# Optimization experiments

Hardware: AMD Instinct MI355X
Metric: run time of the kernel (lower is better)

Reference implementation:

```python
import jax, jax.numpy as jnp
import numpy as np

NH = 8          # num_heads (init kwarg)
NUM_GROUPS = 32
EPS = 1e-5


def setup_inputs() -> dict:
    key = jax.random.key(0)
    ks = jax.random.split(key, 4)
    B, C, H, W = 2, 512, 64, 64
    x = jax.random.normal(ks[0], (B, C, H, W), dtype=jnp.float32)
    qkv_w = jax.random.normal(ks[1], (3 * C, C), dtype=jnp.float32) * (1.0 / np.sqrt(C))
    proj_w = jax.random.normal(ks[2], (C, C), dtype=jnp.float32) * (1.0 / np.sqrt(C))
    proj_b = jax.random.normal(ks[3], (C,), dtype=jnp.float32) * 0.02
    gn_w = jnp.ones((C,), dtype=jnp.float32)
    gn_b = jnp.zeros((C,), dtype=jnp.float32)
    return {"x": x, "qkv_w": qkv_w, "proj_w": proj_w, "proj_b": proj_b,
            "gn_w": gn_w, "gn_b": gn_b}


def _group_norm(x, gamma, beta):
    B, C, H, W = x.shape
    xg = x.reshape(B, NUM_GROUPS, C // NUM_GROUPS, H, W)
    mean = xg.mean(axis=(2, 3, 4), keepdims=True)
    var = xg.var(axis=(2, 3, 4), keepdims=True)
    xg = (xg - mean) * jax.lax.rsqrt(var + EPS)
    x = xg.reshape(B, C, H, W)
    return x * gamma[None, :, None, None] + beta[None, :, None, None]


def reference(x, qkv_w, proj_w, proj_b, gn_w, gn_b):
    B, C, H, W = x.shape
    h = _group_norm(x, gn_w, gn_b)
    # 1x1 conv == channel matmul
    qkv = jnp.einsum('oc,bchw->bohw', qkv_w, h)  # [B, 3C, H, W]
    # faithful legacy reshape: per-head contiguous [q,k,v] blocks of 3*C//NH channels
    qkv = qkv.reshape(B * NH, 3 * C // NH, H * W)
    q, k, v = jnp.split(qkv, 3, axis=1)          # each [B*NH, C//NH, HW]
    scale = 1.0 / np.sqrt(np.sqrt(C // NH))
    attn = jnp.einsum('bci,bcj->bij', q * scale, k * scale)  # [B*NH, HW, HW]
    attn = jax.nn.softmax(attn, axis=-1)
    hout = jnp.einsum('bij,bcj->bci', attn, v)   # [B*NH, C//NH, HW]
    hout = hout.reshape(B, C, H, W)
    hout = jnp.einsum('oc,bchw->bohw', proj_w, hout) + proj_b[None, :, None, None]
    return x + hout
```

## Files before the change

### kernel.cpp

```cpp
#include <hip/hip_runtime.h>
#include <math.h>

typedef __attribute__((ext_vector_type(8))) short short8;
typedef __attribute__((ext_vector_type(4))) short short4v;
typedef __attribute__((ext_vector_type(4))) float floatx4;
typedef __attribute__((ext_vector_type(16))) float floatx16;

__device__ __forceinline__ unsigned short f2bf(float f) {
  union { float f; unsigned int u; } v; v.f = f;
  unsigned int r = v.u + 0x7fffu + ((v.u >> 16) & 1u);
  return (unsigned short)(r >> 16);
}

__device__ __forceinline__ float bf2f(unsigned short h) {
  union { unsigned int u; float f; } v; v.u = ((unsigned int)h) << 16;
  return v.f;
}

__device__ __forceinline__ unsigned int pack2(unsigned short a, unsigned short b) {
  return (unsigned int)a | ((unsigned int)b << 16);
}

__device__ __forceinline__ unsigned int rbits(float f) {
  union { float f; unsigned int u; } v; v.f = f;
  return v.u + 0x8000u;
}

__device__ __forceinline__ float fast_exp2(float x) {
#if __has_builtin(__builtin_amdgcn_exp2f)
  return __builtin_amdgcn_exp2f(x);
#else
  return exp2f(x);
#endif
}

__device__ __forceinline__ void async16(const unsigned short* gp, unsigned short* lp) {
  __builtin_amdgcn_global_load_lds(
      (__attribute__((address_space(1))) void*)(gp),
      (__attribute__((address_space(3))) void*)(lp), 16, 0, 0);
}

__global__ void setup_kernel(const float* __restrict__ x, float* __restrict__ stats,
                             const float* __restrict__ qkv_w, unsigned short* __restrict__ wqkv,
                             const float* __restrict__ proj_w, unsigned short* __restrict__ wproj) {
  if (blockIdx.x < 64) {
    int bg = blockIdx.x;
    const float4* p = (const float4*)(x + (size_t)bg * 65536);
    float s = 0.f, ss = 0.f;
    for (int i = threadIdx.x; i < 16384; i += 256) {
      float4 v = p[i];
      s  += v.x + v.y + v.z + v.w;
      ss += v.x*v.x + v.y*v.y + v.z*v.z + v.w*v.w;
    }
    #pragma unroll
    for (int off = 32; off >= 1; off >>= 1) {
      s  += __shfl_xor(s,  off, 64);
      ss += __shfl_xor(ss, off, 64);
    }
    __shared__ float red[2][4];
    int wv = threadIdx.x >> 6;
    if ((threadIdx.x & 63) == 0) { red[0][wv] = s; red[1][wv] = ss; }
    __syncthreads();
    if (threadIdx.x == 0) {
      s  = red[0][0] + red[0][1] + red[0][2] + red[0][3];
      ss = red[1][0] + red[1][1] + red[1][2] + red[1][3];
      float mean = s * (1.f/65536.f);
      float var  = ss * (1.f/65536.f) - mean*mean;
      stats[2*bg]   = mean;
      stats[2*bg+1] = rsqrtf(var + 1e-5f);
    }
  } else {
    int i = (blockIdx.x - 64) * 256 + threadIdx.x;
    const float* s; unsigned short* d;
    if (i < 196608) { s = qkv_w; d = wqkv; }
    else { i -= 196608; s = proj_w; d = wproj; }
    float4 vv = ((const float4*)s)[i];
    uint2 o;
    o.x = pack2(f2bf(vv.x), f2bf(vv.y));
    o.y = pack2(f2bf(vv.z), f2bf(vv.w));
    ((uint2*)d)[i] = o;
  }
}

__global__ void gn_apply_t(const float* __restrict__ x, const float* __restrict__ stats,
                           const float* __restrict__ gw, const float* __restrict__ gb,
                           unsigned short* __restrict__ h_t) {
  __shared__ __align__(16) unsigned short tile[64][72];
  const int b = blockIdx.z, c0 = blockIdx.y * 64, hw0 = blockIdx.x * 64;
  const int t = threadIdx.x;
  {
    const int cl = t >> 2;
    const int hs = (t & 3) * 16;
    const int c  = c0 + cl;
    const int g  = c >> 4;
    const float mean = stats[2*(b*32 + g)];
    const float rstd = stats[2*(b*32 + g) + 1];
    const float w  = gw[c] * rstd;
    const float bb = gb[c] - mean * w;
    const float4* src = (const float4*)(x + ((size_t)(b*512 + c))*4096 + hw0 + hs);
    #pragma unroll
    for (int i = 0; i < 4; i++) {
      float4 vv = src[i];
      unsigned short* d = &tile[cl][hs + i*4];
      d[0] = f2bf(vv.x*w + bb); d[1] = f2bf(vv.y*w + bb);
      d[2] = f2bf(vv.z*w + bb); d[3] = f2bf(vv.w*w + bb);
    }
  }
  __syncthreads();
  {
    const int hwl = t >> 2;
    const int cs  = (t & 3) * 16;
    uint4 w0, w1;
    w0.x = pack2(tile[cs+ 0][hwl], tile[cs+ 1][hwl]);
    w0.y = pack2(tile[cs+ 2][hwl], tile[cs+ 3][hwl]);
    w0.z = pack2(tile[cs+ 4][hwl], tile[cs+ 5][hwl]);
    w0.w = pack2(tile[cs+ 6][hwl], tile[cs+ 7][hwl]);
    w1.x = pack2(tile[cs+ 8][hwl], tile[cs+ 9][hwl]);
    w1.y = pack2(tile[cs+10][hwl], tile[cs+11][hwl]);
    w1.z = pack2(tile[cs+12][hwl], tile[cs+13][hwl]);
    w1.w = pack2(tile[cs+14][hwl], tile[cs+15][hwl]);
    unsigned short* dst = h_t + ((size_t)(b*4096 + hw0 + hwl))*512 + c0 + cs;
    *(uint4*)dst       = w0;
    *(uint4*)(dst + 8) = w1;
  }
}

__global__ __launch_bounds__(256, 3)
void qkv_gemm(const unsigned short* __restrict__ A,
              const unsigned short* __restrict__ Bt,
              unsigned short* __restrict__ q_t,
              unsigned short* __restrict__ k_t,
              unsigned short* __restrict__ v_) {
  __shared__ __align__(16) unsigned short As[128*32];
  __shared__ __align__(16) unsigned short Bs[128*32];
  const int b   = blockIdx.z;
  const int n0  = blockIdx.x * 128;
  const int o0  = blockIdx.y * 128;
  const int tid = threadIdx.x;
  const int wave = tid >> 6, lane = tid & 63;
  const int wr = wave >> 1, wc = wave & 1;
  const int fm = lane & 15, fq = lane >> 4;
  const int srow = lane >> 2, scol = (lane & 3) * 8;

  const unsigned short* Ab = A + (size_t)o0 * 512;
  const unsigned short* Bb = Bt + ((size_t)b*4096 + n0) * 512;

  bool vsw[4];
  #pragma unroll
  for (int fr = 0; fr < 4; fr++) {
    const int ob = o0 + wr*64 + fr*16;
    vsw[fr] = ((ob % 192) >> 6) == 2;
  }

  floatx4 acc[4][4];
  #pragma unroll
  for (int i = 0; i < 4; i++)
    #pragma unroll
    for (int j = 0; j < 4; j++) acc[i][j] = (floatx4){0.f,0.f,0.f,0.f};

  for (int k0 = 0; k0 < 512; k0 += 32) {
    __syncthreads();
    #pragma unroll
    for (int cc = 0; cc < 2; cc++) {
      int ch = wave*2 + cc;
      async16(Ab + (size_t)(ch*16 + srow)*512 + k0 + scol, &As[ch*512]);
      async16(Bb + (size_t)(ch*16 + srow)*512 + k0 + scol, &Bs[ch*512]);
    }
    __syncthreads();
    short8 af[4], bf[4];
    #pragma unroll
    for (int f = 0; f < 4; f++) {
      af[f] = *(const short8*)&As[(wr*64 + f*16 + fm)*32 + fq*8];
      bf[f] = *(const short8*)&Bs[(wc*64 + f*16 + fm)*32 + fq*8];
    }
    #pragma unroll
    for (int fr = 0; fr < 4; fr++) {
      if (vsw[fr]) {
        #pragma unroll
        for (int fc = 0; fc < 4; fc++)
          acc[fr][fc] = __builtin_amdgcn_mfma_f32_16x16x32_bf16(bf[fc], af[fr], acc[fr][fc], 0, 0, 0);
      } else {
        #pragma unroll
        for (int fc = 0; fc < 4; fc++)
          acc[fr][fc] = __builtin_amdgcn_mfma_f32_16x16x32_bf16(af[fr], bf[fc], acc[fr][fc], 0, 0, 0);
      }
    }
  }

  #pragma unroll
  for (int fr = 0; fr < 4; fr++) {
    const int ob     = o0 + wr*64 + fr*16;
    const int head   = ob / 192;
    const int rem    = ob % 192;
    const int region = rem >> 6;
    const int bhh    = b*8 + head;
    #pragma unroll
    for (int fc = 0; fc < 4; fc++) {
      if (region == 0) {
        const int i = n0 + wc*64 + fc*16 + fm;
        const int dsub = (rem & 63) + fq*4;
        unsigned short t4[4];
        #pragma unroll
        for (int r = 0; r < 4; r++) t4[r] = f2bf(acc[fr][fc][r] * 0.18033688f);
        uint2 o; o.x = pack2(t4[0], t4[1]); o.y = pack2(t4[2], t4[3]);
        *(uint2*)&q_t[((size_t)bhh*4096 + i)*64 + dsub] = o;
      } else if (region == 1) {
        const int i = n0 + wc*64 + fc*16 + fm;
        const int dsub = (rem & 63) + fq*4;
        unsigned short t4[4];
        #pragma unroll
        for (int r = 0; r < 4; r++) t4[r] = f2bf(acc[fr][fc][r]);
        uint2 o; o.x = pack2(t4[0], t4[1]); o.y = pack2(t4[2], t4[3]);
        *(uint2*)&k_t[((size_t)bhh*4096 + i)*64 + dsub] = o;
      } else {
        const int dsub = (rem & 63) + fm;
        const int tok0 = n0 + wc*64 + fc*16 + fq*4;
        unsigned short t4[4];
        #pragma unroll
        for (int r = 0; r < 4; r++) t4[r] = f2bf(acc[fr][fc][r]);
        uint2 o; o.x = pack2(t4[0], t4[1]); o.y = pack2(t4[2], t4[3]);
        *(uint2*)&v_[((size_t)bhh*64 + dsub)*4096 + tok0] = o;
      }
    }
  }
}

__global__ __launch_bounds__(256, 2)
void proj_gemm(const unsigned short* __restrict__ A,
               const unsigned short* __restrict__ Bt,
               float* __restrict__ outp,
               const float* __restrict__ xres,
               const float* __restrict__ pbias) {
  __shared__ __align__(16) unsigned short As[64*32];
  __shared__ __align__(16) unsigned short Bs[128*32];
  const int b   = blockIdx.z;
  const int n0  = blockIdx.x * 128;
  const int o0  = blockIdx.y * 64;
  const int tid = threadIdx.x;
  const int wave = tid >> 6, lane = tid & 63;
  const int wr = wave >> 1, wc = wave & 1;
  const int fm = lane & 15, fq = lane >> 4;
  const int srow = lane >> 2, scol = (lane & 3) * 8;

  const unsigned short* Ab = A + (size_t)o0 * 512;
  const unsigned short* Bb = Bt + ((size_t)b*4096 + n0) * 512;

  floatx4 acc[2][4];
  #pragma unroll
  for (int i = 0; i < 2; i++)
    #pragma unroll
    for (int j = 0; j < 4; j++) acc[i][j] = (floatx4){0.f,0.f,0.f,0.f};

  for (int k0 = 0; k0 < 512; k0 += 32) {
    __syncthreads();
    async16(Ab + (size_t)(wave*16 + srow)*512 + k0 + scol, &As[wave*512]);
    #pragma unroll
    for (int cc = 0; cc < 2; cc++) {
      int ch = wave*2 + cc;
      async16(Bb + (size_t)(ch*16 + srow)*512 + k0 + scol, &Bs[ch*512]);
    }
    __syncthreads();
    short8 af[2], bf[4];
    #pragma unroll
    for (int f = 0; f < 2; f++)
      af[f] = *(const short8*)&As[(wr*32 + f*16 + fm)*32 + fq*8];
    #pragma unroll
    for (int f = 0; f < 4; f++)
      bf[f] = *(const short8*)&Bs[(wc*64 + f*16 + fm)*32 + fq*8];
    #pragma unroll
    for (int fr = 0; fr < 2; fr++)
      #pragma unroll
      for (int fc = 0; fc < 4; fc++)
        acc[fr][fc] = __builtin_amdgcn_mfma_f32_16x16x32_bf16(af[fr], bf[fc], acc[fr][fc], 0, 0, 0);
  }

  #pragma unroll
  for (int fr = 0; fr < 2; fr++)
    #pragma unroll
    for (int fc = 0; fc < 4; fc++) {
      const int i = n0 + wc*64 + fc*16 + fm;
      #pragma unroll
      for (int r = 0; r < 4; r++) {
        const int o = o0 + wr*32 + fr*16 + fq*4 + r;
        const size_t idx = ((size_t)b*512 + o)*4096 + i;
        outp[idx] = xres[idx] + pbias[o] + acc[fr][fc][r];
      }
    }
}

template <int SPLIT>
__global__ __launch_bounds__(256, 2)
void attn_kernel(const unsigned short* __restrict__ q_t,
                 const unsigned short* __restrict__ k_t,
                 const unsigned short* __restrict__ v_,
                 unsigned short* __restrict__ hout_t,
                 unsigned short* __restrict__ o_part,
                 float* __restrict__ l_part) {
  __shared__ __align__(16) unsigned short Ks[2][64*72];
  __shared__ __align__(16) unsigned short Vs[2][64*72];

  const int bh  = blockIdx.x;
  const int q0  = blockIdx.y * 256;
  const int js  = SPLIT ? blockIdx.z : 0;
  const int nit = SPLIT ? 32 : 64;
  const int jbase = js * 2048;
  const int tid = threadIdx.x;
  const int wave = tid >> 6, lane = tid & 63;
  const int ln = lane & 31, h = lane >> 5;

  short8 qf[2][4];
  #pragma unroll
  for (int ih = 0; ih < 2; ih++) {
    const unsigned short* qrow = q_t + ((size_t)bh*4096 + q0 + wave*64 + ih*32 + ln)*64;
    #pragma unroll
    for (int kc = 0; kc < 4; kc++)
      qf[ih][kc] = *(const short8*)(qrow + kc*16 + h*8);
  }

  const floatx16 z16 = {0.f,0.f,0.f,0.f,0.f,0.f,0.f,0.f,
                        0.f,0.f,0.f,0.f,0.f,0.f,0.f,0.f};
  floatx16 o_acc[2][2];
  #pragma unroll
  for (int ih = 0; ih < 2; ih++) { o_acc[ih][0] = z16; o_acc[ih][1] = z16; }
  float l0 = 0.f, l1 = 0.f;

  const int sr = tid >> 3;
  const int sc = (tid & 7) * 8;
  const int cch = tid & 7;
  const int vpos = ((cch >> 2) * 32) + ((cch & 3) * 4);
  const unsigned short* kbase = k_t + (size_t)bh*262144;
  const unsigned short* vbase = v_  + (size_t)bh*262144;

  uint4 kr0 = *(const uint4*)&kbase[(size_t)(jbase + sr)*64 + sc];
  uint4 kr1 = *(const uint4*)&kbase[(size_t)(jbase + sr + 32)*64 + sc];
  uint4 vr0 = *(const uint4*)&vbase[(size_t)sr*4096 + jbase + sc];
  uint4 vr1 = *(const uint4*)&vbase[(size_t)(sr+32)*4096 + jbase + sc];

  for (int it = 0; it < nit; it++) {
    unsigned short* Kc = Ks[it & 1];
    unsigned short* Vc = Vs[it & 1];
    *(uint4*)&Kc[sr*72 + sc]      = kr0;
    *(uint4*)&Kc[(sr+32)*72 + sc] = kr1;
    *(uint2*)&Vc[sr*72 + vpos]           = *(const uint2*)&vr0;
    *(uint2*)&Vc[sr*72 + vpos + 16]      = *((const uint2*)&vr0 + 1);
    *(uint2*)&Vc[(sr+32)*72 + vpos]      = *(const uint2*)&vr1;
    *(uint2*)&Vc[(sr+32)*72 + vpos + 16] = *((const uint2*)&vr1 + 1);
    __syncthreads();

    {
      const int jn = jbase + (((it + 1) & (nit - 1)) * 64);
      kr0 = *(const uint4*)&kbase[(size_t)(jn + sr)*64 + sc];
      kr1 = *(const uint4*)&kbase[(size_t)(jn + sr + 32)*64 + sc];
      vr0 = *(const uint4*)&vbase[(size_t)sr*4096 + jn + sc];
      vr1 = *(const uint4*)&vbase[(size_t)(sr+32)*4096 + jn + sc];
    }

    #pragma unroll
    for (int mj = 0; mj < 2; mj++) {
      short8 kf[4];
      #pragma unroll
      for (int kc = 0; kc < 4; kc++)
        kf[kc] = *(const short8*)&Kc[(mj*32 + ln)*72 + kc*16 + h*8];
      short8 vv[2][2];
      #pragma unroll
      for (int dn = 0; dn < 2; dn++)
        #pragma unroll
        for (int t2 = 0; t2 < 2; t2++)
          vv[dn][t2] = *(const short8*)&Vc[(dn*32 + ln)*72 + mj*32 + h*16 + t2*8];

      #pragma unroll
      for (int ih = 0; ih < 2; ih++) {
        floatx16 st = __builtin_amdgcn_mfma_f32_32x32x16_bf16(kf[0], qf[ih][0], z16, 0, 0, 0);
        #pragma unroll
        for (int kc = 1; kc < 4; kc++)
          st = __builtin_amdgcn_mfma_f32_32x32x16_bf16(kf[kc], qf[ih][kc], st, 0, 0, 0);

        unsigned pk[8];
        float lacc = 0.f;
        #pragma unroll
        for (int rp = 0; rp < 8; rp++) {
          float p0 = fast_exp2(st[2*rp]);
          float p1 = fast_exp2(st[2*rp + 1]);
          lacc += p0 + p1;
          pk[rp] = __builtin_amdgcn_perm(rbits(p1), rbits(p0), 0x07060302u);
        }
        if (ih) l1 += lacc; else l0 += lacc;

        #pragma unroll
        for (int t2 = 0; t2 < 2; t2++) {
          union { unsigned u[2]; short4v s; } a0, a1;
          a0.u[0] = pk[4*t2];     a0.u[1] = pk[4*t2 + 1];
          a1.u[0] = pk[4*t2 + 2]; a1.u[1] = pk[4*t2 + 3];
          #pragma unroll
          for (int dn = 0; dn < 2; dn++) {
            short4v vlo = __builtin_shufflevector(vv[dn][t2], vv[dn][t2], 0, 1, 2, 3);
            short4v vhi = __builtin_shufflevector(vv[dn][t2], vv[dn][t2], 4, 5, 6, 7);
            o_acc[ih][dn] = __builtin_amdgcn_mfma_f32_32x32x8bf16_1k(a0.s, vlo, o_acc[ih][dn], 0, 0, 0);
            o_acc[ih][dn] = __builtin_amdgcn_mfma_f32_32x32x8bf16_1k(a1.s, vhi, o_acc[ih][dn], 0, 0, 0);
          }
        }
      }
    }
  }

  l0 += __shfl_xor(l0, 32, 64);
  l1 += __shfl_xor(l1, 32, 64);

  if (SPLIT) {
    #pragma unroll
    for (int ih = 0; ih < 2; ih++) {
      unsigned short* op = o_part +
          (((size_t)(js*16 + bh)*4096 + q0 + wave*64 + ih*32) * 64);
      #pragma unroll
      for (int r = 0; r < 16; r++) {
        const int il = (r & 3) + 8*(r >> 2) + 4*h;
        op[(size_t)il*64 + ln]      = f2bf(o_acc[ih][0][r]);
        op[(size_t)il*64 + 32 + ln] = f2bf(o_acc[ih][1][r]);
      }
    }
    if (lane < 32) {
      l_part[(size_t)(js*16 + bh)*4096 + q0 + wave*64 + lane]      = l0;
      l_part[(size_t)(js*16 + bh)*4096 + q0 + wave*64 + 32 + lane] = l1;
    }
  } else {
    const float linv0 = 1.f / l0;
    const float linv1 = 1.f / l1;
    const int bb = bh >> 3;
    const int cb = (bh & 7) * 64;
    #pragma unroll
    for (int ih = 0; ih < 2; ih++) {
      #pragma unroll
      for (int r = 0; r < 16; r++) {
        const int il = (r & 3) + 8*(r >> 2) + 4*h;
        const float inv = __shfl(ih ? linv1 : linv0, il, 64);
        const int i = q0 + wave*64 + ih*32 + il;
        unsigned short* dst = &hout_t[((size_t)bb*4096 + i)*512 + cb + ln];
        dst[0]  = f2bf(o_acc[ih][0][r] * inv);
        dst[32] = f2bf(o_acc[ih][1][r] * inv);
      }
    }
  }
}

__global__ void attn_combine(const unsigned short* __restrict__ o_part,
                             const float* __restrict__ l_part,
                             unsigned short* __restrict__ hout_t) {
  const int bh = blockIdx.x;
  const int i0 = blockIdx.y * 64;
  const int t  = threadIdx.x;
  const int d4 = (t & 15) * 4;
  const int il = t >> 4;
  const int bb = bh >> 3;
  const int cb = (bh & 7) * 64;
  const size_t JS = (size_t)16 * 4096 * 64;
  #pragma unroll
  for (int p = 0; p < 4; p++) {
    const int i = i0 + p*16 + il;
    const size_t ob = ((size_t)bh*4096 + i)*64 + d4;
    uint2 a = *(const uint2*)&o_part[ob];
    uint2 b = *(const uint2*)&o_part[ob + JS];
    const size_t lb = (size_t)bh*4096 + i;
    const float inv = 1.f / (l_part[lb] + l_part[lb + 65536]);
    float o0 = (bf2f((unsigned short)(a.x & 0xffff)) + bf2f((unsigned short)(b.x & 0xffff))) * inv;
    float o1 = (bf2f((unsigned short)(a.x >> 16))    + bf2f((unsigned short)(b.x >> 16)))    * inv;
    float o2 = (bf2f((unsigned short)(a.y & 0xffff)) + bf2f((unsigned short)(b.y & 0xffff))) * inv;
    float o3 = (bf2f((unsigned short)(a.y >> 16))    + bf2f((unsigned short)(b.y >> 16)))    * inv;
    uint2 w;
    w.x = pack2(f2bf(o0), f2bf(o1));
    w.y = pack2(f2bf(o2), f2bf(o3));
    *(uint2*)&hout_t[((size_t)bb*4096 + i)*512 + cb + d4] = w;
  }
}

extern "C" void kernel_launch(void* const* d_in, const int* in_sizes, int n_in,
                              void* d_out, int out_size, void* d_ws, size_t ws_size,
                              hipStream_t stream) {
  (void)in_sizes; (void)n_in; (void)out_size;
  const float* x      = (const float*)d_in[0];
  const float* qkv_w  = (const float*)d_in[1];
  const float* proj_w = (const float*)d_in[2];
  const float* proj_b = (const float*)d_in[3];
  const float* gn_w   = (const float*)d_in[4];
  const float* gn_b   = (const float*)d_in[5];
  float* out = (float*)d_out;

  char* ws = (char*)d_ws;
  unsigned short* h_t   = (unsigned short*)(ws);
  unsigned short* q_t   = (unsigned short*)(ws + ((size_t)8  << 20));
  unsigned short* k_t   = (unsigned short*)(ws + ((size_t)16 << 20));
  unsigned short* v_    = (unsigned short*)(ws + ((size_t)24 << 20));
  unsigned short* wqkv  = (unsigned short*)(ws + ((size_t)32 << 20));
  unsigned short* wproj = (unsigned short*)(ws + ((size_t)34 << 20));
  float* stats          = (float*)(ws + ((size_t)35 << 20));
  unsigned short* o_part = (unsigned short*)(ws + ((size_t)36 << 20));
  float* l_part          = (float*)(ws + ((size_t)52 << 20));
  unsigned short* hout_t = h_t;

  const bool split = ws_size >= (((size_t)52 << 20) + ((size_t)1 << 19));

  setup_kernel<<<dim3(1088), dim3(256), 0, stream>>>(x, stats, qkv_w, wqkv, proj_w, wproj);
  gn_apply_t<<<dim3(64, 8, 2), dim3(256), 0, stream>>>(x, stats, gn_w, gn_b, h_t);
  qkv_gemm<<<dim3(32, 12, 2), dim3(256), 0, stream>>>(wqkv, h_t, q_t, k_t, v_);
  if (split) {
    attn_kernel<1><<<dim3(16, 16, 2), dim3(256), 0, stream>>>(q_t, k_t, v_, nullptr,
                                                              o_part, l_part);
    attn_combine<<<dim3(16, 64), dim3(256), 0, stream>>>(o_part, l_part, hout_t);
  } else {
    attn_kernel<0><<<dim3(16, 16), dim3(256), 0, stream>>>(q_t, k_t, v_, hout_t,
                                                           nullptr, nullptr);
  }
  proj_gemm<<<dim3(32, 8, 2), dim3(256), 0, stream>>>(wproj, hout_t, out, x, proj_b);
}
```

Measured before the change: 227.1 us.

## Fuse split-KV attention combine into projection GEMM and raise split count

Removes the separate attn_combine kernel and the non-split attention path. The projection GEMM now reads the partial attention outputs and row sums directly, sums the splits and normalizes while staging its B tile into LDS, and prefetches the next tile's partials into registers. The attention kernel now takes its split count from the grid, using 4 KV splits when the workspace is large enough, and its launch bounds are raised to 4 blocks per CU. This saves one kernel launch and one round-trip of hout through memory, and more splits give more parallel attention blocks. The cost is more partial-output traffic and extra combine work repeated across the 8 output-channel blocks of the projection.

After: 446.3 us. 1.97x slower.

```diff
diff --git a/kernel.cpp b/kernel.cpp
--- a/kernel.cpp
+++ b/kernel.cpp
@@ -12,9 +12,11 @@
   return (unsigned short)(r >> 16);
 }
 
-__device__ __forceinline__ float bf2f(unsigned short h) {
-  union { unsigned int u; float f; } v; v.u = ((unsigned int)h) << 16;
-  return v.f;
+__device__ __forceinline__ float lo16f(unsigned int w) {
+  union { unsigned int u; float f; } v; v.u = w << 16; return v.f;
+}
+__device__ __forceinline__ float hi16f(unsigned int w) {
+  union { unsigned int u; float f; } v; v.u = w & 0xffff0000u; return v.f;
 }
 
 __device__ __forceinline__ unsigned int pack2(unsigned short a, unsigned short b) {
@@ -225,75 +227,10 @@
   }
 }
 
-__global__ __launch_bounds__(256, 2)
-void proj_gemm(const unsigned short* __restrict__ A,
-               const unsigned short* __restrict__ Bt,
-               float* __restrict__ outp,
-               const float* __restrict__ xres,
-               const float* __restrict__ pbias) {
-  __shared__ __align__(16) unsigned short As[64*32];
-  __shared__ __align__(16) unsigned short Bs[128*32];
-  const int b   = blockIdx.z;
-  const int n0  = blockIdx.x * 128;
-  const int o0  = blockIdx.y * 64;
-  const int tid = threadIdx.x;
-  const int wave = tid >> 6, lane = tid & 63;
-  const int wr = wave >> 1, wc = wave & 1;
-  const int fm = lane & 15, fq = lane >> 4;
-  const int srow = lane >> 2, scol = (lane & 3) * 8;
-
-  const unsigned short* Ab = A + (size_t)o0 * 512;
-  const unsigned short* Bb = Bt + ((size_t)b*4096 + n0) * 512;
-
-  floatx4 acc[2][4];
-  #pragma unroll
-  for (int i = 0; i < 2; i++)
-    #pragma unroll
-    for (int j = 0; j < 4; j++) acc[i][j] = (floatx4){0.f,0.f,0.f,0.f};
-
-  for (int k0 = 0; k0 < 512; k0 += 32) {
-    __syncthreads();
-    async16(Ab + (size_t)(wave*16 + srow)*512 + k0 + scol, &As[wave*512]);
-    #pragma unroll
-    for (int cc = 0; cc < 2; cc++) {
-      int ch = wave*2 + cc;
-      async16(Bb + (size_t)(ch*16 + srow)*512 + k0 + scol, &Bs[ch*512]);
-    }
-    __syncthreads();
-    short8 af[2], bf[4];
-    #pragma unroll
-    for (int f = 0; f < 2; f++)
-      af[f] = *(const short8*)&As[(wr*32 + f*16 + fm)*32 + fq*8];
-    #pragma unroll
-    for (int f = 0; f < 4; f++)
-      bf[f] = *(const short8*)&Bs[(wc*64 + f*16 + fm)*32 + fq*8];
-    #pragma unroll
-    for (int fr = 0; fr < 2; fr++)
-      #pragma unroll
-      for (int fc = 0; fc < 4; fc++)
-        acc[fr][fc] = __builtin_amdgcn_mfma_f32_16x16x32_bf16(af[fr], bf[fc], acc[fr][fc], 0, 0, 0);
-  }
-
-  #pragma unroll
-  for (int fr = 0; fr < 2; fr++)
-    #pragma unroll
-    for (int fc = 0; fc < 4; fc++) {
-      const int i = n0 + wc*64 + fc*16 + fm;
-      #pragma unroll
-      for (int r = 0; r < 4; r++) {
-        const int o = o0 + wr*32 + fr*16 + fq*4 + r;
-        const size_t idx = ((size_t)b*512 + o)*4096 + i;
-        outp[idx] = xres[idx] + pbias[o] + acc[fr][fc][r];
-      }
-    }
-}
-
-template <int SPLIT>
-__global__ __launch_bounds__(256, 2)
+__global__ __launch_bounds__(256, 4)
 void attn_kernel(const unsigned short* __restrict__ q_t,
                  const unsigned short* __restrict__ k_t,
                  const unsigned short* __restrict__ v_,
-                 unsigned short* __restrict__ hout_t,
                  unsigned short* __restrict__ o_part,
                  float* __restrict__ l_part) {
   __shared__ __align__(16) unsigned short Ks[2][64*72];
@@ -301,9 +238,9 @@
 
   const int bh  = blockIdx.x;
   const int q0  = blockIdx.y * 256;
-  const int js  = SPLIT ? blockIdx.z : 0;
-  const int nit = SPLIT ? 32 : 64;
-  const int jbase = js * 2048;
+  const int js  = blockIdx.z;
+  const int nit = 64 / gridDim.z;
+  const int jbase = js * nit * 64;
   const int tid = threadIdx.x;
   const int wave = tid >> 6, lane = tid & 63;
   const int ln = lane & 31, h = lane >> 5;
@@ -406,70 +343,145 @@
   l0 += __shfl_xor(l0, 32, 64);
   l1 += __shfl_xor(l1, 32, 64);
 
-  if (SPLIT) {
-    #pragma unroll
-    for (int ih = 0; ih < 2; ih++) {
-      unsigned short* op = o_part +
-          (((size_t)(js*16 + bh)*4096 + q0 + wave*64 + ih*32) * 64);
-      #pragma unroll
-      for (int r = 0; r < 16; r++) {
-        const int il = (r & 3) + 8*(r >> 2) + 4*h;
-        op[(size_t)il*64 + ln]      = f2bf(o_acc[ih][0][r]);
-        op[(size_t)il*64 + 32 + ln] = f2bf(o_acc[ih][1][r]);
+  #pragma unroll
+  for (int ih = 0; ih < 2; ih++) {
+    unsigned short* op = o_part +
+        (((size_t)(js*16 + bh)*4096 + q0 + wave*64 + ih*32) * 64);
+    #pragma unroll
+    for (int r = 0; r < 16; r++) {
+      const int il = (r & 3) + 8*(r >> 2) + 4*h;
+      op[(size_t)il*64 + ln]      = f2bf(o_acc[ih][0][r]);
+      op[(size_t)il*64 + 32 + ln] = f2bf(o_acc[ih][1][r]);
+    }
+  }
+  if (lane < 32) {
+    l_part[(size_t)(js*16 + bh)*4096 + q0 + wave*64 + lane]      = l0;
+    l_part[(size_t)(js*16 + bh)*4096 + q0 + wave*64 + 32 + lane] = l1;
+  }
+}
+
+template <int NS>
+__global__ __launch_bounds__(256, 2)
+void proj_fused(const unsigned short* __restrict__ A,
+                const unsigned short* __restrict__ o_part,
+                const float* __restrict__ l_part,
+                float* __restrict__ outp,
+                const float* __restrict__ xres,
+                const float* __restrict__ pbias) {
+  __shared__ __align__(16) unsigned short As[64*32];
+  __shared__ __align__(16) unsigned short Bs[128*36];
+  __shared__ float Linv[8][128];
+  const int b   = blockIdx.z;
+  const int n0  = blockIdx.x * 128;
+  const int o0  = blockIdx.y * 64;
+  const int tid = threadIdx.x;
+  const int wave = tid >> 6, lane = tid & 63;
+  const int wr = wave >> 1, wc = wave & 1;
+  const int fm = lane & 15, fq = lane >> 4;
+  const int srow = lane >> 2, scol = (lane & 3) * 8;
+  const int tk = tid & 127, hc = tid >> 7;
+
+  #pragma unroll
+  for (int p = 0; p < 4; p++) {
+    const int e = p*256 + tid;
+    const int head = e >> 7, token = e & 127;
+    float s = 0.f;
+    #pragma unroll
+    for (int sp = 0; sp < NS; sp++)
+      s += l_part[((size_t)(sp*16 + b*8 + head)*4096) + n0 + token];
+    Linv[head][token] = 1.f / s;
+  }
+
+  const unsigned short* Ab = A + (size_t)o0 * 512;
+
+  floatx4 acc[2][4];
+  #pragma unroll
+  for (int i = 0; i < 2; i++)
+    #pragma unroll
+    for (int j = 0; j < 4; j++) acc[i][j] = (floatx4){0.f,0.f,0.f,0.f};
+
+  uint4 raw[NS][2];
+  {
+    const int d0 = hc*16;
+    #pragma unroll
+    for (int sp = 0; sp < NS; sp++) {
+      const unsigned short* p = o_part +
+          ((size_t)(sp*16 + b*8)*4096 + n0 + tk)*64 + d0;
+      raw[sp][0] = *(const uint4*)p;
+      raw[sp][1] = *(const uint4*)(p + 8);
+    }
+  }
+
+  for (int k0 = 0; k0 < 512; k0 += 32) {
+    __syncthreads();
+    {
+      const int head = k0 >> 6;
+      const float linv = Linv[head][tk];
+      float fa[16];
+      #pragma unroll
+      for (int j = 0; j < 8; j++) {
+        unsigned w = ((const unsigned*)raw[0])[j];
+        fa[2*j]   = lo16f(w);
+        fa[2*j+1] = hi16f(w);
       }
-    }
-    if (lane < 32) {
-      l_part[(size_t)(js*16 + bh)*4096 + q0 + wave*64 + lane]      = l0;
-      l_part[(size_t)(js*16 + bh)*4096 + q0 + wave*64 + 32 + lane] = l1;
-    }
-  } else {
-    const float linv0 = 1.f / l0;
-    const float linv1 = 1.f / l1;
-    const int bb = bh >> 3;
-    const int cb = (bh & 7) * 64;
-    #pragma unroll
-    for (int ih = 0; ih < 2; ih++) {
-      #pragma unroll
-      for (int r = 0; r < 16; r++) {
-        const int il = (r & 3) + 8*(r >> 2) + 4*h;
-        const float inv = __shfl(ih ? linv1 : linv0, il, 64);
-        const int i = q0 + wave*64 + ih*32 + il;
-        unsigned short* dst = &hout_t[((size_t)bb*4096 + i)*512 + cb + ln];
-        dst[0]  = f2bf(o_acc[ih][0][r] * inv);
-        dst[32] = f2bf(o_acc[ih][1][r] * inv);
+      #pragma unroll
+      for (int sp = 1; sp < NS; sp++)
+        #pragma unroll
+        for (int j = 0; j < 8; j++) {
+          unsigned w = ((const unsigned*)raw[sp])[j];
+          fa[2*j]   += lo16f(w);
+          fa[2*j+1] += hi16f(w);
+        }
+      uint4 o[2];
+      #pragma unroll
+      for (int j = 0; j < 8; j++)
+        ((unsigned*)o)[j] = __builtin_amdgcn_perm(
+            rbits(fa[2*j+1] * linv), rbits(fa[2*j] * linv), 0x07060302u);
+      *(uint4*)&Bs[tk*36 + hc*16]     = o[0];
+      *(uint4*)&Bs[tk*36 + hc*16 + 8] = o[1];
+    }
+    async16(Ab + (size_t)(wave*16 + srow)*512 + k0 + scol, &As[wave*512]);
+    __syncthreads();
+
+    if (k0 + 32 < 512) {
+      const int kn = k0 + 32;
+      const int head = kn >> 6;
+      const int d0 = (kn & 63) + hc*16;
+      #pragma unroll
+      for (int sp = 0; sp < NS; sp++) {
+        const unsigned short* p = o_part +
+            ((size_t)(sp*16 + b*8 + head)*4096 + n0 + tk)*64 + d0;
+        raw[sp][0] = *(const uint4*)p;
+        raw[sp][1] = *(const uint4*)(p + 8);
       }
     }
-  }
-}
-
-__global__ void attn_combine(const unsigned short* __restrict__ o_part,
-                             const float* __restrict__ l_part,
-                             unsigned short* __restrict__ hout_t) {
-  const int bh = blockIdx.x;
-  const int i0 = blockIdx.y * 64;
-  const int t  = threadIdx.x;
-  const int d4 = (t & 15) * 4;
-  const int il = t >> 4;
-  const int bb = bh >> 3;
-  const int cb = (bh & 7) * 64;
-  const size_t JS = (size_t)16 * 4096 * 64;
-  #pragma unroll
-  for (int p = 0; p < 4; p++) {
-    const int i = i0 + p*16 + il;
-    const size_t ob = ((size_t)bh*4096 + i)*64 + d4;
-    uint2 a = *(const uint2*)&o_part[ob];
-    uint2 b = *(const uint2*)&o_part[ob + JS];
-    const size_t lb = (size_t)bh*4096 + i;
-    const float inv = 1.f / (l_part[lb] + l_part[lb + 65536]);
-    float o0 = (bf2f((unsigned short)(a.x & 0xffff)) + bf2f((unsigned short)(b.x & 0xffff))) * inv;
-    float o1 = (bf2f((unsigned short)(a.x >> 16))    + bf2f((unsigned short)(b.x >> 16)))    * inv;
-    float o2 = (bf2f((unsigned short)(a.y & 0xffff)) + bf2f((unsigned short)(b.y & 0xffff))) * inv;
-    float o3 = (bf2f((unsigned short)(a.y >> 16))    + bf2f((unsigned short)(b.y >> 16)))    * inv;
-    uint2 w;
-    w.x = pack2(f2bf(o0), f2bf(o1));
-    w.y = pack2(f2bf(o2), f2bf(o3));
-    *(uint2*)&hout_t[((size_t)bb*4096 + i)*512 + cb + d4] = w;
-  }
+
+    short8 af[2], bf[4];
+    #pragma unroll
+    for (int f = 0; f < 2; f++)
+      af[f] = *(const short8*)&As[(wr*32 + f*16 + fm)*32 + fq*8];
+    #pragma unroll
+    for (int f = 0; f < 4; f++)
+      bf[f] = *(const short8*)&Bs[(wc*64 + f*16 + fm)*36 + fq*8];
+    #pragma unroll
+    for (int fr = 0; fr < 2; fr++)
+      #pragma unroll
+      for (int fc = 0; fc < 4; fc++)
+        acc[fr][fc] = __builtin_amdgcn_mfma_f32_16x16x32_bf16(af[fr], bf[fc], acc[fr][fc], 0, 0, 0);
+  }
+
+  #pragma unroll
+  for (int fr = 0; fr < 2; fr++)
+    #pragma unroll
+    for (int fc = 0; fc < 4; fc++) {
+      const int i = n0 + wc*64 + fc*16 + fm;
+      #pragma unroll
+      for (int r = 0; r < 4; r++) {
+        const int o = o0 + wr*32 + fr*16 + fq*4 + r;
+        const size_t idx = ((size_t)b*512 + o)*4096 + i;
+        outp[idx] = xres[idx] + pbias[o] + acc[fr][fc][r];
+      }
+    }
 }
 
 extern "C" void kernel_launch(void* const* d_in, const int* in_sizes, int n_in,
@@ -493,21 +505,18 @@
   unsigned short* wproj = (unsigned short*)(ws + ((size_t)34 << 20));
   float* stats          = (float*)(ws + ((size_t)35 << 20));
   unsigned short* o_part = (unsigned short*)(ws + ((size_t)36 << 20));
-  float* l_part          = (float*)(ws + ((size_t)52 << 20));
-  unsigned short* hout_t = h_t;
-
-  const bool split = ws_size >= (((size_t)52 << 20) + ((size_t)1 << 19));
+
+  const int ns = (ws_size >= ((size_t)70 << 20)) ? 4 : 2;
+  float* l_part = (float*)(ws + ((size_t)36 << 20) + (size_t)ns * (8 << 20));
 
   setup_kernel<<<dim3(1088), dim3(256), 0, stream>>>(x, stats, qkv_w, wqkv, proj_w, wproj);
   gn_apply_t<<<dim3(64, 8, 2), dim3(256), 0, stream>>>(x, stats, gn_w, gn_b, h_t);
   qkv_gemm<<<dim3(32, 12, 2), dim3(256), 0, stream>>>(wqkv, h_t, q_t, k_t, v_);
-  if (split) {
-    attn_kernel<1><<<dim3(16, 16, 2), dim3(256), 0, stream>>>(q_t, k_t, v_, nullptr,
-                                                              o_part, l_part);
-    attn_combine<<<dim3(16, 64), dim3(256), 0, stream>>>(o_part, l_part, hout_t);
-  } else {
-    attn_kernel<0><<<dim3(16, 16), dim3(256), 0, stream>>>(q_t, k_t, v_, hout_t,
-                                                           nullptr, nullptr);
-  }
-  proj_gemm<<<dim3(32, 8, 2), dim3(256), 0, stream>>>(wproj, hout_t, out, x, proj_b);
-}
+  attn_kernel<<<dim3(16, 16, ns), dim3(256), 0, stream>>>(q_t, k_t, v_, o_part, l_part);
+  if (ns == 4)
+    proj_fused<4><<<dim3(32, 8, 2), dim3(256), 0, stream>>>(wproj, o_part, l_part,
+                                                            out, x, proj_b);
+  else
+    proj_fused<2><<<dim3(32, 8, 2), dim3(256), 0, stream>>>(wproj, o_part, l_part,
+                                                            out, x, proj_b);
+}
```

## Drop split-KV attention and combine kernel; use 128-thread blocks with full key loop

Applied to the files above, without the earlier changes.

Removes the two-way key split and its attn_combine pass. Each attention block now processes all 4096 keys with 2 waves over 128 queries, writing normalized output straight into hout_t. This avoids writing bf16 partial outputs and l sums, re-reading them, and paying an extra kernel launch. In exchange, each K/V tile staged in LDS is shared by only 2 waves instead of 4. There are also half as many waves in flight, each running twice as many iterations, which lowers occupancy and latency hiding.

New measurement: 278.0 us. 1.22x slower.

```diff
diff --git a/kernel.cpp b/kernel.cpp
--- a/kernel.cpp
+++ b/kernel.cpp
@@ -10,11 +10,6 @@
   union { float f; unsigned int u; } v; v.f = f;
   unsigned int r = v.u + 0x7fffu + ((v.u >> 16) & 1u);
   return (unsigned short)(r >> 16);
-}
-
-__device__ __forceinline__ float bf2f(unsigned short h) {
-  union { unsigned int u; float f; } v; v.u = ((unsigned int)h) << 16;
-  return v.f;
 }
 
 __device__ __forceinline__ unsigned int pack2(unsigned short a, unsigned short b) {
@@ -288,22 +283,16 @@
     }
 }
 
-template <int SPLIT>
-__global__ __launch_bounds__(256, 2)
+__global__ __launch_bounds__(128, 2)
 void attn_kernel(const unsigned short* __restrict__ q_t,
                  const unsigned short* __restrict__ k_t,
                  const unsigned short* __restrict__ v_,
-                 unsigned short* __restrict__ hout_t,
-                 unsigned short* __restrict__ o_part,
-                 float* __restrict__ l_part) {
+                 unsigned short* __restrict__ hout_t) {
   __shared__ __align__(16) unsigned short Ks[2][64*72];
   __shared__ __align__(16) unsigned short Vs[2][64*72];
 
   const int bh  = blockIdx.x;
-  const int q0  = blockIdx.y * 256;
-  const int js  = SPLIT ? blockIdx.z : 0;
-  const int nit = SPLIT ? 32 : 64;
-  const int jbase = js * 2048;
+  const int q0  = blockIdx.y * 128;
   const int tid = threadIdx.x;
   const int wave = tid >> 6, lane = tid & 63;
   const int ln = lane & 31, h = lane >> 5;
@@ -331,28 +320,32 @@
   const unsigned short* kbase = k_t + (size_t)bh*262144;
   const unsigned short* vbase = v_  + (size_t)bh*262144;
 
-  uint4 kr0 = *(const uint4*)&kbase[(size_t)(jbase + sr)*64 + sc];
-  uint4 kr1 = *(const uint4*)&kbase[(size_t)(jbase + sr + 32)*64 + sc];
-  uint4 vr0 = *(const uint4*)&vbase[(size_t)sr*4096 + jbase + sc];
-  uint4 vr1 = *(const uint4*)&vbase[(size_t)(sr+32)*4096 + jbase + sc];
-
-  for (int it = 0; it < nit; it++) {
+  uint4 kr[4], vr[4];
+  #pragma unroll
+  for (int p = 0; p < 4; p++) {
+    kr[p] = *(const uint4*)&kbase[(size_t)(sr + 16*p)*64 + sc];
+    vr[p] = *(const uint4*)&vbase[(size_t)(sr + 16*p)*4096 + sc];
+  }
+
+  for (int it = 0; it < 64; it++) {
     unsigned short* Kc = Ks[it & 1];
     unsigned short* Vc = Vs[it & 1];
-    *(uint4*)&Kc[sr*72 + sc]      = kr0;
-    *(uint4*)&Kc[(sr+32)*72 + sc] = kr1;
-    *(uint2*)&Vc[sr*72 + vpos]           = *(const uint2*)&vr0;
-    *(uint2*)&Vc[sr*72 + vpos + 16]      = *((const uint2*)&vr0 + 1);
-    *(uint2*)&Vc[(sr+32)*72 + vpos]      = *(const uint2*)&vr1;
-    *(uint2*)&Vc[(sr+32)*72 + vpos + 16] = *((const uint2*)&vr1 + 1);
+    #pragma unroll
+    for (int p = 0; p < 4; p++) {
+      const int row = sr + 16*p;
+      *(uint4*)&Kc[row*72 + sc] = kr[p];
+      *(uint2*)&Vc[row*72 + vpos]      = *(const uint2*)&vr[p];
+      *(uint2*)&Vc[row*72 + vpos + 16] = *((const uint2*)&vr[p] + 1);
+    }
     __syncthreads();
 
     {
-      const int jn = jbase + (((it + 1) & (nit - 1)) * 64);
-      kr0 = *(const uint4*)&kbase[(size_t)(jn + sr)*64 + sc];
-      kr1 = *(const uint4*)&kbase[(size_t)(jn + sr + 32)*64 + sc];
-      vr0 = *(const uint4*)&vbase[(size_t)sr*4096 + jn + sc];
-      vr1 = *(const uint4*)&vbase[(size_t)(sr+32)*4096 + jn + sc];
+      const int jn = ((it + 1) & 63) * 64;
+      #pragma unroll
+      for (int p = 0; p < 4; p++) {
+        kr[p] = *(const uint4*)&kbase[(size_t)(jn + sr + 16*p)*64 + sc];
+        vr[p] = *(const uint4*)&vbase[(size_t)(sr + 16*p)*4096 + jn + sc];
+      }
     }
 
     #pragma unroll
@@ -405,77 +398,28 @@
 
   l0 += __shfl_xor(l0, 32, 64);
   l1 += __shfl_xor(l1, 32, 64);
-
-  if (SPLIT) {
-    #pragma unroll
-    for (int ih = 0; ih < 2; ih++) {
-      unsigned short* op = o_part +
-          (((size_t)(js*16 + bh)*4096 + q0 + wave*64 + ih*32) * 64);
-      #pragma unroll
-      for (int r = 0; r < 16; r++) {
-        const int il = (r & 3) + 8*(r >> 2) + 4*h;
-        op[(size_t)il*64 + ln]      = f2bf(o_acc[ih][0][r]);
-        op[(size_t)il*64 + 32 + ln] = f2bf(o_acc[ih][1][r]);
-      }
-    }
-    if (lane < 32) {
-      l_part[(size_t)(js*16 + bh)*4096 + q0 + wave*64 + lane]      = l0;
-      l_part[(size_t)(js*16 + bh)*4096 + q0 + wave*64 + 32 + lane] = l1;
-    }
-  } else {
-    const float linv0 = 1.f / l0;
-    const float linv1 = 1.f / l1;
-    const int bb = bh >> 3;
-    const int cb = (bh & 7) * 64;
-    #pragma unroll
-    for (int ih = 0; ih < 2; ih++) {
-      #pragma unroll
-      for (int r = 0; r < 16; r++) {
-        const int il = (r & 3) + 8*(r >> 2) + 4*h;
-        const float inv = __shfl(ih ? linv1 : linv0, il, 64);
-        const int i = q0 + wave*64 + ih*32 + il;
-        unsigned short* dst = &hout_t[((size_t)bb*4096 + i)*512 + cb + ln];
-        dst[0]  = f2bf(o_acc[ih][0][r] * inv);
-        dst[32] = f2bf(o_acc[ih][1][r] * inv);
-      }
-    }
-  }
-}
-
-__global__ void attn_combine(const unsigned short* __restrict__ o_part,
-                             const float* __restrict__ l_part,
-                             unsigned short* __restrict__ hout_t) {
-  const int bh = blockIdx.x;
-  const int i0 = blockIdx.y * 64;
-  const int t  = threadIdx.x;
-  const int d4 = (t & 15) * 4;
-  const int il = t >> 4;
+  const float linv0 = 1.f / l0;
+  const float linv1 = 1.f / l1;
   const int bb = bh >> 3;
   const int cb = (bh & 7) * 64;
-  const size_t JS = (size_t)16 * 4096 * 64;
-  #pragma unroll
-  for (int p = 0; p < 4; p++) {
-    const int i = i0 + p*16 + il;
-    const size_t ob = ((size_t)bh*4096 + i)*64 + d4;
-    uint2 a = *(const uint2*)&o_part[ob];
-    uint2 b = *(const uint2*)&o_part[ob + JS];
-    const size_t lb = (size_t)bh*4096 + i;
-    const float inv = 1.f / (l_part[lb] + l_part[lb + 65536]);
-    float o0 = (bf2f((unsigned short)(a.x & 0xffff)) + bf2f((unsigned short)(b.x & 0xffff))) * inv;
-    float o1 = (bf2f((unsigned short)(a.x >> 16))    + bf2f((unsigned short)(b.x >> 16)))    * inv;
-    float o2 = (bf2f((unsigned short)(a.y & 0xffff)) + bf2f((unsigned short)(b.y & 0xffff))) * inv;
-    float o3 = (bf2f((unsigned short)(a.y >> 16))    + bf2f((unsigned short)(b.y >> 16)))    * inv;
-    uint2 w;
-    w.x = pack2(f2bf(o0), f2bf(o1));
-    w.y = pack2(f2bf(o2), f2bf(o3));
-    *(uint2*)&hout_t[((size_t)bb*4096 + i)*512 + cb + d4] = w;
+  #pragma unroll
+  for (int ih = 0; ih < 2; ih++) {
+    #pragma unroll
+    for (int r = 0; r < 16; r++) {
+      const int il = (r & 3) + 8*(r >> 2) + 4*h;
+      const float inv = __shfl(ih ? linv1 : linv0, il, 64);
+      const int i = q0 + wave*64 + ih*32 + il;
+      unsigned short* dst = &hout_t[((size_t)bb*4096 + i)*512 + cb + ln];
+      dst[0]  = f2bf(o_acc[ih][0][r] * inv);
+      dst[32] = f2bf(o_acc[ih][1][r] * inv);
+    }
   }
 }
 
 extern "C" void kernel_launch(void* const* d_in, const int* in_sizes, int n_in,
                               void* d_out, int out_size, void* d_ws, size_t ws_size,
                               hipStream_t stream) {
-  (void)in_sizes; (void)n_in; (void)out_size;
+  (void)in_sizes; (void)n_in; (void)out_size; (void)ws_size;
   const float* x      = (const float*)d_in[0];
   const float* qkv_w  = (const float*)d_in[1];
   const float* proj_w = (const float*)d_in[2];
@@ -492,22 +436,11 @@
   unsigned short* wqkv  = (unsigned short*)(ws + ((size_t)32 << 20));
   unsigned short* wproj = (unsigned short*)(ws + ((size_t)34 << 20));
   float* stats          = (float*)(ws + ((size_t)35 << 20));
-  unsigned short* o_part = (unsigned short*)(ws + ((size_t)36 << 20));
-  float* l_part          = (float*)(ws + ((size_t)52 << 20));
   unsigned short* hout_t = h_t;
-
-  const bool split = ws_size >= (((size_t)52 << 20) + ((size_t)1 << 19));
 
   setup_kernel<<<dim3(1088), dim3(256), 0, stream>>>(x, stats, qkv_w, wqkv, proj_w, wproj);
   gn_apply_t<<<dim3(64, 8, 2), dim3(256), 0, stream>>>(x, stats, gn_w, gn_b, h_t);
   qkv_gemm<<<dim3(32, 12, 2), dim3(256), 0, stream>>>(wqkv, h_t, q_t, k_t, v_);
-  if (split) {
-    attn_kernel<1><<<dim3(16, 16, 2), dim3(256), 0, stream>>>(q_t, k_t, v_, nullptr,
-                                                              o_part, l_part);
-    attn_combine<<<dim3(16, 64), dim3(256), 0, stream>>>(o_part, l_part, hout_t);
-  } else {
-    attn_kernel<0><<<dim3(16, 16), dim3(256), 0, stream>>>(q_t, k_t, v_, hout_t,
-                                                           nullptr, nullptr);
-  }
+  attn_kernel<<<dim3(16, 32), dim3(128), 0, stream>>>(q_t, k_t, v_, hout_t);
   proj_gemm<<<dim3(32, 8, 2), dim3(256), 0, stream>>>(wproj, hout_t, out, x, proj_b);
 }
```
